# Kernel tuning notes

Hardware: AMD Instinct MI355X
Metric: run time of the kernel (lower is better)

## Reference

```python
import jax, jax.numpy as jnp
import numpy as np

PATCH = 14          # config.patch_size
MAX_SEQ = 2048      # config.max_vit_seq_len
A2 = 4              # adaptor_patch_size ** 2
GRID = 32           # max_image_size // patch_size -> sqrt(num_positions - 1)
EPS = 1e-5          # layer_norm_eps

IMG_SIZES = [(448, 448), (448, 672), (336, 336), (224, 448), (560, 560), (336, 448)]


def bilinear_resize_chw(img, oh, ow):
    # torch F.interpolate(mode='bilinear', align_corners=False): half-pixel centers, edge clamp
    C, H, W = img.shape
    def coords(o, i):
        c = (jnp.arange(o, dtype=jnp.float32) + 0.5) * (i / o) - 0.5
        c = jnp.clip(c, 0.0, i - 1.0)
        lo = jnp.floor(c).astype(jnp.int32)
        hi = jnp.minimum(lo + 1, i - 1)
        return lo, hi, c - lo
    y0, y1, wy = coords(oh, H)
    x0, x1, wx = coords(ow, W)
    top = img[:, y0][:, :, x0] * (1 - wx) + img[:, y0][:, :, x1] * wx
    bot = img[:, y1][:, :, x0] * (1 - wx) + img[:, y1][:, :, x1] * wx
    wy = wy[None, :, None]
    return top * (1 - wy) + bot * wy


def patch_embed(img, conv_w, conv_b):
    # Conv2d(k=stride=PATCH) == non-overlapping patch extract + matmul
    C, H, W = img.shape
    h, w = H // PATCH, W // PATCH
    x = img[:, :h * PATCH, :w * PATCH].reshape(C, h, PATCH, w, PATCH)
    x = x.transpose(1, 3, 0, 2, 4).reshape(h * w, C * PATCH * PATCH)  # [hw, c*kh*kw]
    out = x @ conv_w.reshape(conv_w.shape[0], -1).T + conv_b          # [hw, E]
    return out, (h, w)


def pos_embed_interp(pos_table, h, w):
    pe = pos_table[1:]  # drop cls position, [GRID*GRID, E]
    if (h, w) == (GRID, GRID):
        return pe
    E = pe.shape[-1]
    pe2d = pe.reshape(GRID, GRID, E).transpose(2, 0, 1)  # [E, GRID, GRID]
    pe2d = bilinear_resize_chw(pe2d, h, w)
    return pe2d.transpose(1, 2, 0).reshape(h * w, E)


def layernorm(x, g, b):
    m = x.mean(-1, keepdims=True)
    v = ((x - m) ** 2).mean(-1, keepdims=True)
    return (x - m) / jnp.sqrt(v + EPS) * g + b


def pack_positions(hw_list):
    # static replay of group_images_by_max_seq_len + a2 rescale in forward
    pos, batch_idx, seq_len = [], 0, 0
    for (h, w) in hw_list:
        L = h * w
        if seq_len + L > MAX_SEQ:
            batch_idx += 1
            seq_len = 0
        s = (seq_len // A2) * A2
        pos.append((batch_idx, s, s + (L // A2) * A2))
        seq_len += L
    return pos, batch_idx + 1


def setup_inputs() -> dict:
    key = jax.random.key(0)
    ks = jax.random.split(key, 9)
    E = 1280
    inp = {}
    for i, (H, W) in enumerate(IMG_SIZES):
        inp[f'img{i}'] = jax.random.normal(ks[i], (3, H, W), dtype=jnp.float32)
    inp['conv_w'] = jax.random.normal(ks[6], (E, 3, PATCH, PATCH), dtype=jnp.float32) * 0.02
    inp['conv_b'] = jnp.zeros((E,), dtype=jnp.float32)
    inp['pos_table'] = jax.random.normal(ks[7], (GRID * GRID + 1, E), dtype=jnp.float32) * 0.02
    inp['ln_w'] = jnp.ones((E,), dtype=jnp.float32)
    inp['ln_b'] = jnp.zeros((E,), dtype=jnp.float32)
    return inp


def reference(img0, img1, img2, img3, img4, img5, conv_w, conv_b, pos_table, ln_w, ln_b):
    images = [img0, img1, img2, img3, img4, img5]
    E = conv_w.shape[0]
    hw = [(im.shape[1] // PATCH, im.shape[2] // PATCH) for im in images]
    positions, B = pack_positions(hw)
    emb = jnp.zeros((B, MAX_SEQ, E), dtype=jnp.float32)
    mask = np.zeros((B, 1, MAX_SEQ, MAX_SEQ), dtype=bool)
    for im, (bi, s, e) in zip(images, positions):
        x, (h, w) = patch_embed(im, conv_w, conv_b)
        x = x + pos_embed_interp(pos_table, h, w)
        x = layernorm(x, ln_w, ln_b)
        emb = emb.at[bi, s:e].set(x)
        mask[bi, 0, s:e, s:e] = True
    return emb, jnp.asarray(mask)
```

## Files before the change

kernel.cpp:

```cpp
#include <hip/hip_runtime.h>
#include <hip/hip_bf16.h>
#include <stdint.h>

#define E_DIM 1280
#define KDIM 588
#define KPAD 608
#define M_TOTAL 6016
#define EMB_FLOATS (5*2048*1280)
#define MASK_FLOATS (5*2048*2048)

#define EXT_BLOCKS  3572
#define CW_BLOCKS   760
#define PREP_BLOCKS (EXT_BLOCKS + CW_BLOCKS)

#define GEMM_BLOCKS 188
#define ZERO_BLOCKS2 660
#define MASK_BLOCKS2 2560
#define FUSED_BLOCKS (GEMM_BLOCKS + ZERO_BLOCKS2 + MASK_BLOCKS2)

typedef __attribute__((ext_vector_type(8))) short bf16x8;
typedef __attribute__((ext_vector_type(4))) float f32x4;

struct us4 { unsigned short x, y, z, w; };

__device__ __forceinline__ unsigned short f2bf(float f) {
    unsigned int u = __float_as_uint(f);
    u += 0x7fff + ((u >> 16) & 1);
    return (unsigned short)(u >> 16);
}

template<int PW, int IMGW, int PLANE>
__device__ __forceinline__ void do_extract4(const float* __restrict__ img,
                                            us4* __restrict__ A4,
                                            int base_u4, int local_u4)
{
    int r_local = local_u4 / 152;
    int k4 = (local_u4 - r_local * 152) * 4;
    us4 v = {0, 0, 0, 0};
    if (k4 < KDIM) {
        int py = r_local / PW;  int px = r_local - py * PW;
        int c   = k4 / 196;
        int rem0 = k4 - c * 196;
        const float* p = img + (size_t)c * PLANE;
        unsigned short o[4];
        #pragma unroll
        for (int j = 0; j < 4; ++j) {
            int rem = rem0 + j;
            int iy = rem / 14, ix = rem - iy * 14;
            o[j] = f2bf(p[(size_t)(py*14 + iy) * IMGW + (px*14 + ix)]);
        }
        v.x = o[0]; v.y = o[1]; v.z = o[2]; v.w = o[3];
    }
    A4[base_u4 + local_u4] = v;
}

__global__ __launch_bounds__(256) void prep(
    const float* __restrict__ i0, const float* __restrict__ i1,
    const float* __restrict__ i2, const float* __restrict__ i3,
    const float* __restrict__ i4, const float* __restrict__ i5,
    const float* __restrict__ conv_w,
    us4* __restrict__ A4, us4* __restrict__ W4)
{
    const int bid = blockIdx.x;
    const int t = threadIdx.x;
    if (bid < EXT_BLOCKS) {
        if (bid < 608) {
            do_extract4<32,448,200704>(i0, A4, 0,      bid * 256 + t);
        } else if (bid < 1520) {
            do_extract4<48,672,301056>(i1, A4, 155648, (bid - 608) * 256 + t);
        } else if (bid < 1862) {
            do_extract4<24,336,112896>(i2, A4, 389120, (bid - 1520) * 256 + t);
        } else if (bid < 2166) {
            do_extract4<32,448,100352>(i3, A4, 476672, (bid - 1862) * 256 + t);
        } else if (bid < 3116) {
            do_extract4<40,560,313600>(i4, A4, 554496, (bid - 2166) * 256 + t);
        } else {
            do_extract4<32,448,150528>(i5, A4, 797696, (bid - 3116) * 256 + t);
        }
    } else {
        int idx4 = (bid - EXT_BLOCKS) * 256 + t;
        int e  = idx4 / 152;
        int k4 = (idx4 - e * 152) * 4;
        us4 v = {0, 0, 0, 0};
        if (k4 < KDIM) {
            const float* p = conv_w + (size_t)e * KDIM + k4;
            v.x = f2bf(p[0]); v.y = f2bf(p[1]); v.z = f2bf(p[2]); v.w = f2bf(p[3]);
        }
        W4[idx4] = v;
    }
}

__global__ __launch_bounds__(512) void fused_gemm(
    const unsigned short* __restrict__ A,
    const unsigned short* __restrict__ Wb,
    const float* __restrict__ pos_table, const float* __restrict__ conv_b,
    const float* __restrict__ ln_w, const float* __restrict__ ln_b,
    float* __restrict__ out, float4* __restrict__ out4)
{
    const int bid = blockIdx.x;
    const int t = threadIdx.x;

    if (bid < GEMM_BLOCKS) {
        const int m0   = bid * 32;
        const int wave = t >> 6;
        const int lane = t & 63;
        const int l16  = lane & 15, q = lane >> 4;
        const int ncol0 = wave * 160;

        f32x4 acc[2][10] = {};
        const unsigned short* ap = A  + (size_t)(m0 + l16) * KPAD + q * 8;
        const unsigned short* bp = Wb + (size_t)(ncol0 + l16) * KPAD + q * 8;

        bf16x8 ab[2][2], bb[2][10];
        #pragma unroll
        for (int mi = 0; mi < 2; ++mi) ab[0][mi] = *(const bf16x8*)(ap + mi * 16 * KPAD);
        #pragma unroll
        for (int ni = 0; ni < 10; ++ni) bb[0][ni] = *(const bf16x8*)(bp + ni * 16 * KPAD);

        #pragma unroll
        for (int kki = 0; kki < 19; ++kki) {
            const int cur = kki & 1, nxt = cur ^ 1;
            if (kki < 18) {
                const unsigned short* apn = ap + (kki + 1) * 32;
                const unsigned short* bpn = bp + (kki + 1) * 32;
                #pragma unroll
                for (int mi = 0; mi < 2; ++mi) ab[nxt][mi] = *(const bf16x8*)(apn + mi * 16 * KPAD);
                #pragma unroll
                for (int ni = 0; ni < 10; ++ni) bb[nxt][ni] = *(const bf16x8*)(bpn + ni * 16 * KPAD);
            }
            #pragma unroll
            for (int mi = 0; mi < 2; ++mi)
                #pragma unroll
                for (int ni = 0; ni < 10; ++ni)
                    acc[mi][ni] = __builtin_amdgcn_mfma_f32_16x16x32_bf16(
                        ab[cur][mi], bb[cur][ni], acc[mi][ni], 0, 0, 0);
        }

        int img     = (m0 < 1024) ? 0 : (m0 < 2560) ? 1 : (m0 < 3136) ? 2 : (m0 < 3648) ? 3 : (m0 < 5248) ? 4 : 5;
        int rowOff  = (img == 0) ? 0 : (img == 1) ? 1024 : (img == 2) ? 2560 : (img == 3) ? 3136 : (img == 4) ? 3648 : 5248;
        int h       = (img == 0) ? 32 : (img == 1) ? 32 : (img == 2) ? 24 : (img == 3) ? 16 : (img == 4) ? 40 : 24;
        int w       = (img == 0) ? 32 : (img == 1) ? 48 : (img == 2) ? 24 : (img == 3) ? 32 : (img == 4) ? 40 : 32;
        int outBase = (img == 0) ? 0 : (img == 1) ? 2048 : (img == 2) ? 4096 : (img == 3) ? 4672 : (img == 4) ? 6144 : 8192;
        unsigned int magic = (unsigned int)((1u << 22) / (unsigned)w) + 1u;
        float sh = 32.0f / (float)h, sw = 32.0f / (float)w;

        float cbv[10], gv[10], bev[10];
        #pragma unroll
        for (int ni = 0; ni < 10; ++ni) {
            int col = ncol0 + ni * 16 + l16;
            cbv[ni] = conv_b[col];
            gv[ni]  = ln_w[col];
            bev[ni] = ln_b[col];
        }

        __shared__ float part_s[8][32], part_s2[8][32], ln_m[32], ln_i[32];

        #pragma unroll
        for (int mi = 0; mi < 2; ++mi) {
            #pragma unroll
            for (int reg = 0; reg < 4; ++reg) {
                int row_t = mi * 16 + q * 4 + reg;
                int ri = m0 + row_t - rowOff;
                unsigned int y = ((unsigned int)ri * magic) >> 22;
                int x = ri - (int)y * w;
                float cy = fminf(fmaxf(((float)y + 0.5f) * sh - 0.5f, 0.0f), 31.0f);
                float cx = fminf(fmaxf(((float)x + 0.5f) * sw - 0.5f, 0.0f), 31.0f);
                int y0 = (int)cy; int y1 = min(y0 + 1, 31); float wy = cy - (float)y0;
                int x0 = (int)cx; int x1 = min(x0 + 1, 31); float wx = cx - (float)x0;
                float w00 = (1.f - wy) * (1.f - wx), w01 = (1.f - wy) * wx;
                float w10 = wy * (1.f - wx),         w11 = wy * wx;
                const float* P00 = pos_table + (size_t)(1 + y0*32 + x0) * E_DIM;
                const float* P01 = pos_table + (size_t)(1 + y0*32 + x1) * E_DIM;
                const float* P10 = pos_table + (size_t)(1 + y1*32 + x0) * E_DIM;
                const float* P11 = pos_table + (size_t)(1 + y1*32 + x1) * E_DIM;
                float s = 0.f, s2 = 0.f;
                #pragma unroll
                for (int ni = 0; ni < 10; ++ni) {
                    int col = ncol0 + ni * 16 + l16;
                    float p = w00*P00[col] + w01*P01[col] + w10*P10[col] + w11*P11[col];
                    float v = acc[mi][ni][reg] + cbv[ni] + p;
                    acc[mi][ni][reg] = v;
                    s += v; s2 += v * v;
                }
                #pragma unroll
                for (int msk = 1; msk < 16; msk <<= 1) {
                    s  += __shfl_xor(s,  msk, 64);
                    s2 += __shfl_xor(s2, msk, 64);
                }
                if (l16 == 0) { part_s[wave][row_t] = s; part_s2[wave][row_t] = s2; }
            }
        }
        __syncthreads();
        if (t < 32) {
            float S = 0.f, S2 = 0.f;
            #pragma unroll
            for (int w2 = 0; w2 < 8; ++w2) { S += part_s[w2][t]; S2 += part_s2[w2][t]; }
            float mean = S / 1280.f;
            float var  = S2 / 1280.f - mean * mean;
            ln_m[t] = mean;
            ln_i[t] = 1.f / sqrtf(var + 1e-5f);
        }
        __syncthreads();

        #pragma unroll
        for (int mi = 0; mi < 2; ++mi) {
            #pragma unroll
            for (int reg = 0; reg < 4; ++reg) {
                int row_t = mi * 16 + q * 4 + reg;
                int ri = m0 + row_t - rowOff;
                float mean = ln_m[row_t], inv = ln_i[row_t];
                float* orow = out + (size_t)(outBase + ri) * E_DIM;
                #pragma unroll
                for (int ni = 0; ni < 10; ++ni) {
                    int col = ncol0 + ni * 16 + l16;
                    orow[col] = (acc[mi][ni][reg] - mean) * inv * gv[ni] + bev[ni];
                }
            }
        }
    } else if (bid < GEMM_BLOCKS + ZERO_BLOCKS2) {
        int base = (bid - GEMM_BLOCKS) * 2048 + t;
        #pragma unroll
        for (int j = 0; j < 4; ++j) {
            int idx = base + j * 512;
            int zrow = idx / 320;
            int c4   = idx - zrow * 320;
            int b, rowInB;
            if      (zrow < 1024) { b = 0; rowInB = 1024 + zrow; }
            else if (zrow < 1536) { b = 1; rowInB = 1536 + (zrow - 1024); }
            else if (zrow < 2496) { b = 2; rowInB = 1088 + (zrow - 1536); }
            else if (zrow < 2944) { b = 3; rowInB = 1600 + (zrow - 2496); }
            else                  { b = 4; rowInB =  768 + (zrow - 2944); }
            size_t o4 = ((size_t)(b * 2048 + rowInB) * E_DIM) / 4 + c4;
            out4[o4] = make_float4(0.f, 0.f, 0.f, 0.f);
        }
    } else {
        int base = (bid - GEMM_BLOCKS - ZERO_BLOCKS2) * 2048 + t;
        #pragma unroll
        for (int j = 0; j < 4; ++j) {
            int m4 = base + j * 512;
            int b  = m4 >> 20;
            int rr = (m4 >> 9) & 2047;
            int c0 = (m4 & 511) * 4;
            int h0 = (b == 0) ? 1024 : (b == 1) ? 1536 : (b == 2) ? 576 : (b == 3) ? 1600 : 768;
            bool on = (rr < h0 && c0 < h0);
            if (b == 2) on = on || (rr >= 576 && rr < 1088 && c0 >= 576 && c0 < 1088);
            float f = on ? 1.f : 0.f;
            out4[(size_t)(EMB_FLOATS / 4) + m4] = make_float4(f, f, f, f);
        }
    }
}

extern "C" void kernel_launch(void* const* d_in, const int* in_sizes, int n_in,
                              void* d_out, int out_size, void* d_ws, size_t ws_size,
                              hipStream_t stream) {
    const float* img0 = (const float*)d_in[0];
    const float* img1 = (const float*)d_in[1];
    const float* img2 = (const float*)d_in[2];
    const float* img3 = (const float*)d_in[3];
    const float* img4 = (const float*)d_in[4];
    const float* img5 = (const float*)d_in[5];
    const float* conv_w    = (const float*)d_in[6];
    const float* conv_b    = (const float*)d_in[7];
    const float* pos_table = (const float*)d_in[8];
    const float* ln_w      = (const float*)d_in[9];
    const float* ln_b      = (const float*)d_in[10];
    float* out = (float*)d_out;

    unsigned short* Abf = (unsigned short*)d_ws;
    unsigned short* Wbf = Abf + (size_t)M_TOTAL * KPAD;

    prep<<<PREP_BLOCKS, 256, 0, stream>>>(
        img0, img1, img2, img3, img4, img5, conv_w, (us4*)Abf, (us4*)Wbf);

    fused_gemm<<<FUSED_BLOCKS, 512, 0, stream>>>(
        Abf, Wbf, pos_table, conv_b, ln_w, ln_b, out, (float4*)out);
}
```

Before: 204.0 us.

## Fuse patch extraction into GEMM via shared-memory A tile

Patch extraction and bf16 conversion of the image pixels move out of the prep kernel and into the GEMM blocks, which now write a 32-row A tile straight into LDS. The A operand is then read from shared memory instead of a global workspace buffer. This removes the global write and read-back of the ~7MB bf16 A matrix and shrinks the prep launch to weight conversion only. In exchange, each GEMM block pays uncoalesced strided image gathers before its MFMA loop, and LDS use grows, which may reduce occupancy.

```diff
diff --git a/kernel.cpp b/kernel.cpp
--- a/kernel.cpp
+++ b/kernel.cpp
@@ -5,13 +5,11 @@
 #define E_DIM 1280
 #define KDIM 588
 #define KPAD 608
+#define ALD  616
 #define M_TOTAL 6016
 #define EMB_FLOATS (5*2048*1280)
-#define MASK_FLOATS (5*2048*2048)
-
-#define EXT_BLOCKS  3572
-#define CW_BLOCKS   760
-#define PREP_BLOCKS (EXT_BLOCKS + CW_BLOCKS)
+
+#define PREP_BLOCKS 760
 
 #define GEMM_BLOCKS 188
 #define ZERO_BLOCKS2 660
@@ -29,69 +27,24 @@
     return (unsigned short)(u >> 16);
 }
 
-template<int PW, int IMGW, int PLANE>
-__device__ __forceinline__ void do_extract4(const float* __restrict__ img,
-                                            us4* __restrict__ A4,
-                                            int base_u4, int local_u4)
+__global__ __launch_bounds__(256) void prep_w(
+    const float* __restrict__ conv_w, us4* __restrict__ W4)
 {
-    int r_local = local_u4 / 152;
-    int k4 = (local_u4 - r_local * 152) * 4;
+    int idx4 = blockIdx.x * 256 + threadIdx.x;
+    int e  = idx4 / 152;
+    int k4 = (idx4 - e * 152) * 4;
     us4 v = {0, 0, 0, 0};
     if (k4 < KDIM) {
-        int py = r_local / PW;  int px = r_local - py * PW;
-        int c   = k4 / 196;
-        int rem0 = k4 - c * 196;
-        const float* p = img + (size_t)c * PLANE;
-        unsigned short o[4];
-        #pragma unroll
-        for (int j = 0; j < 4; ++j) {
-            int rem = rem0 + j;
-            int iy = rem / 14, ix = rem - iy * 14;
-            o[j] = f2bf(p[(size_t)(py*14 + iy) * IMGW + (px*14 + ix)]);
-        }
-        v.x = o[0]; v.y = o[1]; v.z = o[2]; v.w = o[3];
+        const float* p = conv_w + (size_t)e * KDIM + k4;
+        v.x = f2bf(p[0]); v.y = f2bf(p[1]); v.z = f2bf(p[2]); v.w = f2bf(p[3]);
     }
-    A4[base_u4 + local_u4] = v;
-}
-
-__global__ __launch_bounds__(256) void prep(
+    W4[idx4] = v;
+}
+
+__global__ __launch_bounds__(512) void fused_gemm(
     const float* __restrict__ i0, const float* __restrict__ i1,
     const float* __restrict__ i2, const float* __restrict__ i3,
     const float* __restrict__ i4, const float* __restrict__ i5,
-    const float* __restrict__ conv_w,
-    us4* __restrict__ A4, us4* __restrict__ W4)
-{
-    const int bid = blockIdx.x;
-    const int t = threadIdx.x;
-    if (bid < EXT_BLOCKS) {
-        if (bid < 608) {
-            do_extract4<32,448,200704>(i0, A4, 0,      bid * 256 + t);
-        } else if (bid < 1520) {
-            do_extract4<48,672,301056>(i1, A4, 155648, (bid - 608) * 256 + t);
-        } else if (bid < 1862) {
-            do_extract4<24,336,112896>(i2, A4, 389120, (bid - 1520) * 256 + t);
-        } else if (bid < 2166) {
-            do_extract4<32,448,100352>(i3, A4, 476672, (bid - 1862) * 256 + t);
-        } else if (bid < 3116) {
-            do_extract4<40,560,313600>(i4, A4, 554496, (bid - 2166) * 256 + t);
-        } else {
-            do_extract4<32,448,150528>(i5, A4, 797696, (bid - 3116) * 256 + t);
-        }
-    } else {
-        int idx4 = (bid - EXT_BLOCKS) * 256 + t;
-        int e  = idx4 / 152;
-        int k4 = (idx4 - e * 152) * 4;
-        us4 v = {0, 0, 0, 0};
-        if (k4 < KDIM) {
-            const float* p = conv_w + (size_t)e * KDIM + k4;
-            v.x = f2bf(p[0]); v.y = f2bf(p[1]); v.z = f2bf(p[2]); v.w = f2bf(p[3]);
-        }
-        W4[idx4] = v;
-    }
-}
-
-__global__ __launch_bounds__(512) void fused_gemm(
-    const unsigned short* __restrict__ A,
     const unsigned short* __restrict__ Wb,
     const float* __restrict__ pos_table, const float* __restrict__ conv_b,
     const float* __restrict__ ln_w, const float* __restrict__ ln_b,
@@ -100,6 +53,9 @@
     const int bid = blockIdx.x;
     const int t = threadIdx.x;
 
+    __shared__ __align__(16) unsigned short Atile[32][ALD];
+    __shared__ float part_s[8][32], part_s2[8][32], ln_m[32], ln_i[32];
+
     if (bid < GEMM_BLOCKS) {
         const int m0   = bid * 32;
         const int wave = t >> 6;
@@ -107,42 +63,68 @@
         const int l16  = lane & 15, q = lane >> 4;
         const int ncol0 = wave * 160;
 
-        f32x4 acc[2][10] = {};
-        const unsigned short* ap = A  + (size_t)(m0 + l16) * KPAD + q * 8;
-        const unsigned short* bp = Wb + (size_t)(ncol0 + l16) * KPAD + q * 8;
-
-        bf16x8 ab[2][2], bb[2][10];
-        #pragma unroll
-        for (int mi = 0; mi < 2; ++mi) ab[0][mi] = *(const bf16x8*)(ap + mi * 16 * KPAD);
-        #pragma unroll
-        for (int ni = 0; ni < 10; ++ni) bb[0][ni] = *(const bf16x8*)(bp + ni * 16 * KPAD);
-
-        #pragma unroll
-        for (int kki = 0; kki < 19; ++kki) {
-            const int cur = kki & 1, nxt = cur ^ 1;
-            if (kki < 18) {
-                const unsigned short* apn = ap + (kki + 1) * 32;
-                const unsigned short* bpn = bp + (kki + 1) * 32;
-                #pragma unroll
-                for (int mi = 0; mi < 2; ++mi) ab[nxt][mi] = *(const bf16x8*)(apn + mi * 16 * KPAD);
-                #pragma unroll
-                for (int ni = 0; ni < 10; ++ni) bb[nxt][ni] = *(const bf16x8*)(bpn + ni * 16 * KPAD);
-            }
-            #pragma unroll
-            for (int mi = 0; mi < 2; ++mi)
-                #pragma unroll
-                for (int ni = 0; ni < 10; ++ni)
-                    acc[mi][ni] = __builtin_amdgcn_mfma_f32_16x16x32_bf16(
-                        ab[cur][mi], bb[cur][ni], acc[mi][ni], 0, 0, 0);
-        }
-
         int img     = (m0 < 1024) ? 0 : (m0 < 2560) ? 1 : (m0 < 3136) ? 2 : (m0 < 3648) ? 3 : (m0 < 5248) ? 4 : 5;
         int rowOff  = (img == 0) ? 0 : (img == 1) ? 1024 : (img == 2) ? 2560 : (img == 3) ? 3136 : (img == 4) ? 3648 : 5248;
         int h       = (img == 0) ? 32 : (img == 1) ? 32 : (img == 2) ? 24 : (img == 3) ? 16 : (img == 4) ? 40 : 24;
         int w       = (img == 0) ? 32 : (img == 1) ? 48 : (img == 2) ? 24 : (img == 3) ? 32 : (img == 4) ? 40 : 32;
         int outBase = (img == 0) ? 0 : (img == 1) ? 2048 : (img == 2) ? 4096 : (img == 3) ? 4672 : (img == 4) ? 6144 : 8192;
+        int IMGW    = (img == 0) ? 448 : (img == 1) ? 672 : (img == 2) ? 336 : (img == 3) ? 448 : (img == 4) ? 560 : 448;
+        int PLANE   = (img == 0) ? 200704 : (img == 1) ? 301056 : (img == 2) ? 112896 : (img == 3) ? 100352 : (img == 4) ? 313600 : 150528;
+        const float* ip = (img == 0) ? i0 : (img == 1) ? i1 : (img == 2) ? i2 : (img == 3) ? i3 : (img == 4) ? i4 : i5;
         unsigned int magic = (unsigned int)((1u << 22) / (unsigned)w) + 1u;
         float sh = 32.0f / (float)h, sw = 32.0f / (float)w;
+
+        #pragma unroll
+        for (int j = 0; j < 10; ++j) {
+            int i = t + j * 512;
+            if (j < 9 || i < 4864) {
+                int r_local = i / 152;
+                int k4 = (i - r_local * 152) * 4;
+                us4 v = {0, 0, 0, 0};
+                if (k4 < KDIM) {
+                    int ri = m0 + r_local - rowOff;
+                    unsigned int py = ((unsigned int)ri * magic) >> 22;
+                    int px = ri - (int)py * w;
+                    int c    = k4 / 196;
+                    int rem0 = k4 - c * 196;
+                    const float* p = ip + (size_t)c * PLANE + (size_t)((int)py * 14) * IMGW + px * 14;
+                    unsigned short o[4];
+                    #pragma unroll
+                    for (int jj = 0; jj < 4; ++jj) {
+                        int rem = rem0 + jj;
+                        int iy = rem / 14, ix = rem - iy * 14;
+                        o[jj] = f2bf(p[(size_t)iy * IMGW + ix]);
+                    }
+                    v.x = o[0]; v.y = o[1]; v.z = o[2]; v.w = o[3];
+                }
+                *(us4*)&Atile[r_local][k4] = v;
+            }
+        }
+
+        const unsigned short* bp = Wb + (size_t)(ncol0 + l16) * KPAD + q * 8;
+        bf16x8 bb[2][10];
+        #pragma unroll
+        for (int ni = 0; ni < 10; ++ni) bb[0][ni] = *(const bf16x8*)(bp + ni * 16 * KPAD);
+
+        __syncthreads();
+
+        f32x4 acc[2][10] = {};
+        #pragma unroll
+        for (int kki = 0; kki < 19; ++kki) {
+            const int cur = kki & 1, nxt = cur ^ 1;
+            if (kki < 18) {
+                const unsigned short* bpn = bp + (kki + 1) * 32;
+                #pragma unroll
+                for (int ni = 0; ni < 10; ++ni) bb[nxt][ni] = *(const bf16x8*)(bpn + ni * 16 * KPAD);
+            }
+            bf16x8 a0 = *(const bf16x8*)&Atile[l16][kki * 32 + q * 8];
+            bf16x8 a1 = *(const bf16x8*)&Atile[16 + l16][kki * 32 + q * 8];
+            #pragma unroll
+            for (int ni = 0; ni < 10; ++ni) {
+                acc[0][ni] = __builtin_amdgcn_mfma_f32_16x16x32_bf16(a0, bb[cur][ni], acc[0][ni], 0, 0, 0);
+                acc[1][ni] = __builtin_amdgcn_mfma_f32_16x16x32_bf16(a1, bb[cur][ni], acc[1][ni], 0, 0, 0);
+            }
+        }
 
         float cbv[10], gv[10], bev[10];
         #pragma unroll
@@ -152,8 +134,6 @@
             gv[ni]  = ln_w[col];
             bev[ni] = ln_b[col];
         }
-
-        __shared__ float part_s[8][32], part_s2[8][32], ln_m[32], ln_i[32];
 
         #pragma unroll
         for (int mi = 0; mi < 2; ++mi) {
@@ -266,12 +246,11 @@
     const float* ln_b      = (const float*)d_in[10];
     float* out = (float*)d_out;
 
-    unsigned short* Abf = (unsigned short*)d_ws;
-    unsigned short* Wbf = Abf + (size_t)M_TOTAL * KPAD;
-
-    prep<<<PREP_BLOCKS, 256, 0, stream>>>(
-        img0, img1, img2, img3, img4, img5, conv_w, (us4*)Abf, (us4*)Wbf);
+    unsigned short* Wbf = (unsigned short*)d_ws;
+
+    prep_w<<<PREP_BLOCKS, 256, 0, stream>>>(conv_w, (us4*)Wbf);
 
     fused_gemm<<<FUSED_BLOCKS, 512, 0, stream>>>(
-        Abf, Wbf, pos_table, conv_b, ln_w, ln_b, out, (float4*)out);
-}
+        img0, img1, img2, img3, img4, img5,
+        Wbf, pos_table, conv_b, ln_w, ln_b, out, (float4*)out);
+}
```

Result: no change. 205.3 us (+0.6%).
